# Performance work log

Measured on AMD Instinct MI355X. Metric: run time of the kernel, lower is better.

## Reference

```python
import jax, jax.numpy as jnp
import numpy as np

N_HEADS = 16


def setup_inputs() -> dict:
    key = jax.random.key(0)
    ks = jax.random.split(key, 6)
    b, s, d = 1, 2048, 2048
    x = jax.random.normal(ks[0], (b, s, d), dtype=jnp.float32)
    Wqkv = jax.random.normal(ks[1], (d, 3 * d), dtype=jnp.float32) * (d ** -0.5)
    Wqkv_bias = jax.random.normal(ks[2], (3 * d,), dtype=jnp.float32) * 0.02
    out_w = jax.random.normal(ks[3], (d, d), dtype=jnp.float32) * (d ** -0.5)
    out_b = jax.random.normal(ks[4], (d,), dtype=jnp.float32) * 0.02
    attn_bias = jax.random.normal(ks[5], (1, N_HEADS, 1, s), dtype=jnp.float32)
    key_padding_mask = jnp.ones((b, s), dtype=bool)
    return {"x": x, "Wqkv": Wqkv, "Wqkv_bias": Wqkv_bias, "out_w": out_w,
            "out_b": out_b, "attn_bias": attn_bias,
            "key_padding_mask": key_padding_mask}


def reference(x, Wqkv, Wqkv_bias, out_w, out_b, attn_bias, key_padding_mask):
    b, s, d = x.shape
    h = N_HEADS
    dh = d // h
    qkv = x @ Wqkv + Wqkv_bias                      # [b, s, 3d]
    q, k, v = jnp.split(qkv, 3, axis=-1)
    q = q.reshape(b, s, h, dh).transpose(0, 2, 1, 3)  # b h s d
    k = k.reshape(b, s, h, dh).transpose(0, 2, 1, 3)
    v = v.reshape(b, s, h, dh).transpose(0, 2, 1, 3)
    scale = 1.0 / jnp.sqrt(jnp.asarray(dh, x.dtype))
    attn_weight = jnp.einsum('bhqd,bhkd->bhqk', q, k) * scale
    attn_weight = attn_weight + attn_bias           # broadcast [1,h,1,s]
    min_val = jnp.finfo(x.dtype).min
    # key padding mask: [b, s_k] -> [b,1,1,s_k]
    attn_weight = jnp.where(key_padding_mask[:, None, None, :], attn_weight, min_val)
    # causal mask (s_q == s_k)
    causal = jnp.tril(jnp.ones((s, s), dtype=bool))
    attn_weight = jnp.where(causal[None, None, :, :], attn_weight, min_val)
    attn_weight = jax.nn.softmax(attn_weight, axis=-1)
    out = jnp.einsum('bhqk,bhkd->bhqd', attn_weight, v)
    out = out.transpose(0, 2, 1, 3).reshape(b, s, d)  # b s (h d)
    return out @ out_w + out_b
```

## Files before the change

kernel.cpp:

```cpp
#include <hip/hip_runtime.h>
#include <hip/hip_bf16.h>
#include <stdint.h>


#define SQ 2048
#define DM 2048
#define NH 16
#define DH 128
#define N3 6144
#define QKVN (NH * SQ * DH)

typedef unsigned short u16;
typedef __bf16 bf16_t;
typedef bf16_t bf16x8 __attribute__((ext_vector_type(8)));
typedef float f32x4 __attribute__((ext_vector_type(4)));
typedef const __attribute__((address_space(1))) unsigned int guint;
typedef __attribute__((address_space(3))) unsigned int luint;

__device__ __forceinline__ float b2f(u16 u) {
    union { uint32_t i; float f; } c; c.i = ((uint32_t)u) << 16; return c.f;
}
__device__ __forceinline__ u16 f2b(float f) {
    union { float f; uint32_t i; } c; c.f = f;
    uint32_t r = c.i + 0x7FFF + ((c.i >> 16) & 1);
    return (u16)(r >> 16);
}
__device__ __forceinline__ uint32_t pk(u16 a, u16 b) {
    return (uint32_t)a | ((uint32_t)b << 16);
}
__device__ __forceinline__ uint32_t pkrnd(float a, float b) {
    union { float f; uint32_t i; } x, y; x.f = a; y.f = b;
    return __builtin_amdgcn_perm(y.i + 0x8000u, x.i + 0x8000u, 0x07060302u);
}
__device__ __forceinline__ float ld1(const void* p, size_t i, bool fp32) {
    return fp32 ? ((const float*)p)[i] : b2f(((const u16*)p)[i]);
}

__global__ void detect_dtype(const void* x, int* flag) {
    __shared__ int bad;
    if (threadIdx.x == 0) bad = 0;
    __syncthreads();
    float v = b2f(((const u16*)x)[threadIdx.x]);
    if (!(fabsf(v) <= 1024.0f)) atomicOr(&bad, 1);
    __syncthreads();
    if (threadIdx.x == 0) *flag = bad;
}

__global__ __launch_bounds__(256) void convert_x(
    const void* __restrict__ x, u16* __restrict__ xb, const int* __restrict__ flagp)
{
    const bool fp32 = (*flagp != 0);
    const size_t i = ((size_t)blockIdx.x * 256 + threadIdx.x) * 8;
    uint4 v;
    if (fp32) {
        const float* p = (const float*)x + i;
        float4 a = *(const float4*)p, b = *(const float4*)(p + 4);
        v.x = pkrnd(a.x, a.y); v.y = pkrnd(a.z, a.w);
        v.z = pkrnd(b.x, b.y); v.w = pkrnd(b.z, b.w);
    } else {
        v = *(const uint4*)((const u16*)x + i);
    }
    *(uint4*)(xb + i) = v;
}

__global__ __launch_bounds__(256) void transpose_w(
    const void* __restrict__ W, u16* __restrict__ Wt, int N,
    const int* __restrict__ flagp)
{
    const bool fp32 = (*flagp != 0);
    __shared__ __attribute__((aligned(16))) u16 tile[64 * 72];
    const int t = threadIdx.x;
    const int n0 = blockIdx.x * 64, k0 = blockIdx.y * 64;
#pragma unroll
    for (int i = 0; i < 2; ++i) {
        int c = t + 256 * i; int kr = c >> 3; int n8 = (c & 7) * 8;
        uint4 v;
        if (fp32) {
            const float* p = (const float*)W + (size_t)(k0 + kr) * N + n0 + n8;
            float4 a = *(const float4*)p, b = *(const float4*)(p + 4);
            v.x = pkrnd(a.x, a.y); v.y = pkrnd(a.z, a.w);
            v.z = pkrnd(b.x, b.y); v.w = pkrnd(b.z, b.w);
        } else {
            v = *(const uint4*)((const u16*)W + (size_t)(k0 + kr) * N + n0 + n8);
        }
        *(uint4*)&tile[kr * 72 + n8] = v;
    }
    __syncthreads();
#pragma unroll
    for (int i = 0; i < 2; ++i) {
        int c = t + 256 * i; int nr = c >> 3; int k8 = (c & 7) * 8;
        uint32_t dw[4];
#pragma unroll
        for (int j = 0; j < 4; ++j)
            dw[j] = pk(tile[(k8 + 2*j) * 72 + nr], tile[(k8 + 2*j + 1) * 72 + nr]);
        *(uint4*)&Wt[(size_t)(n0 + nr) * 2048 + k0 + k8] =
            make_uint4(dw[0], dw[1], dw[2], dw[3]);
    }
}

__global__ __launch_bounds__(256, 2) void qkv_gemm4(
    const u16* __restrict__ xb, const u16* __restrict__ Wt,
    const void* __restrict__ bias,
    u16* __restrict__ Q, u16* __restrict__ K, u16* __restrict__ Vt,
    const int* __restrict__ flagp)
{
    const bool fp32 = (*flagp != 0);
    __shared__ __attribute__((aligned(16))) u16 Alds[2][128 * 64];
    __shared__ __attribute__((aligned(16))) u16 Blds[2][192 * 64];
    const int t = threadIdx.x;
    const int w = t >> 6, l = t & 63;
    const int wm = w >> 1, wn = w & 1;
    const int lq = l & 15, quad = l >> 4;
    const int rsub = t >> 3;
    const int sw = ((t & 7) ^ (rsub & 7)) << 3;

    const int orig = blockIdx.x;
    const int xcd = orig & 7, j = orig >> 3;
    const int bx = (xcd & 3) * 8 + (j & 7);
    const int by = (xcd >> 2) * 8 + (j >> 3);
    const int m0 = by * 128, n0 = bx * 192;

    const u16* Ag = xb + (size_t)m0 * 2048;
    const u16* Bg = Wt + (size_t)n0 * 2048;

#define STAGE_A(u, ue) do {                                                   \
    if ((u) < 32) {                                                           \
      _Pragma("unroll")                                                       \
      for (int i_ = 0; i_ < 2; ++i_) {                                        \
        const int rb_ = i_ * 64 + (ue) * 32;                                  \
        const u16* src_ = Ag + (size_t)(rb_ + rsub) * 2048 + (u) * 64 + sw;   \
        __builtin_amdgcn_global_load_lds((guint*)(const void*)src_,           \
          (luint*)(void*)&Alds[(u) & 1][rb_ * 64 + t * 8], 16, 0, 0);         \
      }                                                                       \
    } } while (0)

#define STAGE_B(u) do {                                                       \
    if ((u) < 32) {                                                           \
      _Pragma("unroll")                                                       \
      for (int i_ = 0; i_ < 6; ++i_) {                                        \
        const int rb_ = i_ * 32;                                              \
        const u16* src_ = Bg + (size_t)(rb_ + rsub) * 2048 + (u) * 64 + sw;   \
        __builtin_amdgcn_global_load_lds((guint*)(const void*)src_,           \
          (luint*)(void*)&Blds[(u) & 1][rb_ * 64 + t * 8], 16, 0, 0);         \
      }                                                                       \
    } } while (0)

#define READ_A(buf, mh) do {                                                  \
    _Pragma("unroll")                                                         \
    for (int mf_ = 0; mf_ < 2; ++mf_) {                                       \
      const int r_ = wm*64 + ((mh)*2 + mf_)*16 + lq;                          \
      _Pragma("unroll")                                                       \
      for (int ks_ = 0; ks_ < 2; ++ks_) {                                     \
        const int c_ = (ks_*4 + quad) ^ (r_ & 7);                             \
        a[mf_][ks_] = *(const bf16x8*)&Alds[buf][r_*64 + c_*8];               \
      }                                                                       \
    } } while (0)

#define READ_B(dst, buf, nhh) do {                                            \
    _Pragma("unroll")                                                         \
    for (int nf_ = 0; nf_ < 3; ++nf_) {                                       \
      const int r_ = wn*96 + ((nhh)*3 + nf_)*16 + lq;                         \
      _Pragma("unroll")                                                       \
      for (int ks_ = 0; ks_ < 2; ++ks_) {                                     \
        const int c_ = (ks_*4 + quad) ^ (r_ & 7);                             \
        dst[nf_][ks_] = *(const bf16x8*)&Blds[buf][r_*64 + c_*8];             \
      }                                                                       \
    } } while (0)

#define MMA_Q(mh, nhh, bsrc) do {                                             \
    __builtin_amdgcn_s_setprio(1);                                            \
    _Pragma("unroll")                                                         \
    for (int mf_ = 0; mf_ < 2; ++mf_)                                         \
    _Pragma("unroll")                                                         \
    for (int nf_ = 0; nf_ < 3; ++nf_)                                         \
    _Pragma("unroll")                                                         \
    for (int ks_ = 0; ks_ < 2; ++ks_)                                         \
      acc[(mh)*2+mf_][(nhh)*3+nf_] =                                          \
        __builtin_amdgcn_mfma_f32_16x16x32_bf16(a[mf_][ks_], bsrc[nf_][ks_],  \
          acc[(mh)*2+mf_][(nhh)*3+nf_], 0, 0, 0);                             \
    __builtin_amdgcn_s_setprio(0);                                            \
} while (0)

#define TILE_BODY(T, buf, BEC, BEN) do {                                      \
                                                                      \
    READ_A(buf, 0);                                                           \
    __builtin_amdgcn_s_barrier();                                             \
    asm volatile("s_waitcnt lgkmcnt(0)" ::: "memory");                        \
    MMA_Q(0, 0, BEC);                                                         \
    __builtin_amdgcn_s_barrier();                                             \
                                                                      \
    READ_B(bo, buf, 1);                                                       \
    STAGE_A((T) + 2, 0);                                                      \
    if ((T) >= 30) asm volatile("s_waitcnt vmcnt(0)" ::: "memory");           \
    else           asm volatile("s_waitcnt vmcnt(2)" ::: "memory");           \
    __builtin_amdgcn_s_barrier();                                             \
    asm volatile("s_waitcnt lgkmcnt(0)" ::: "memory");                        \
    MMA_Q(0, 1, bo);                                                          \
    __builtin_amdgcn_s_barrier();                                             \
                                                                      \
    READ_A(buf, 1);                                                           \
    STAGE_B((T) + 2);                                                         \
    __builtin_amdgcn_s_barrier();                                             \
    asm volatile("s_waitcnt lgkmcnt(0)" ::: "memory");                        \
    MMA_Q(1, 1, bo);                                                          \
    __builtin_amdgcn_s_barrier();                                             \
                                                                      \
    READ_B(BEN, (buf) ^ 1, 0);                                                \
    STAGE_A((T) + 2, 1);                                                      \
    __builtin_amdgcn_s_barrier();                                             \
    asm volatile("s_waitcnt lgkmcnt(0)" ::: "memory");                        \
    MMA_Q(1, 0, BEC);                                                         \
    __builtin_amdgcn_s_barrier();                                             \
} while (0)

    const f32x4 vzero = {0.f, 0.f, 0.f, 0.f};
    f32x4 acc[4][6];
#pragma unroll
    for (int i = 0; i < 4; ++i)
#pragma unroll
        for (int j2 = 0; j2 < 6; ++j2) acc[i][j2] = vzero;
    bf16x8 a[2][2], bo[3][2], be_a[3][2], be_b[3][2];

    STAGE_A(0, 0); STAGE_B(0); STAGE_A(0, 1);
    STAGE_A(1, 0); STAGE_B(1); STAGE_A(1, 1);
    asm volatile("s_waitcnt vmcnt(10)" ::: "memory");
    __builtin_amdgcn_s_barrier();
    READ_B(be_a, 0, 0);

#pragma unroll 1
    for (int T = 0; T < 32; T += 2) {
        TILE_BODY(T,     0, be_a, be_b);
        TILE_BODY(T + 1, 1, be_b, be_a);
    }

    const float scale = 0.08838834764831845f;
#pragma unroll
    for (int nf = 0; nf < 6; ++nf) {
        const int n = n0 + wn*96 + nf*16 + lq;
        const float bn = ld1(bias, n, fp32);
        const int which = n >> 11, r2 = n & 2047, h = r2 >> 7, dc = r2 & 127;
#pragma unroll
        for (int mf = 0; mf < 4; ++mf) {
#pragma unroll
            for (int r = 0; r < 4; ++r) {
                const int m = m0 + wm*64 + mf*16 + quad*4 + r;
                const float val = acc[mf][nf][r] + bn;
                if (which == 0)
                    Q[((size_t)(h << 11) + m) * DH + dc] = f2b(val * scale);
                else if (which == 1)
                    K[((size_t)(h << 11) + m) * DH + dc] = f2b(val);
                else {
                    const int kl = m & 63;
                    const int pos = ((kl >> 5) << 5) + (((kl >> 2) & 3) << 3)
                                  + (((kl >> 4) & 1) << 2) + (kl & 3);
                    const int mp = (m & ~63) | pos;
                    Vt[((size_t)h * DH + dc) * SQ + mp] = f2b(val);
                }
            }
        }
    }
#undef STAGE_A
#undef STAGE_B
#undef READ_A
#undef READ_B
#undef MMA_Q
#undef TILE_BODY
}

__global__ __launch_bounds__(256) void attn_mfma(
    const u16* __restrict__ Q, const u16* __restrict__ K,
    const u16* __restrict__ Vt, const void* __restrict__ attn_bias,
    u16* __restrict__ Ob0, u16* __restrict__ Ob1,
    float* __restrict__ Lb0, float* __restrict__ Lb1,
    const int* __restrict__ flagp)
{
    const bool fp32 = (*flagp != 0);
    __shared__ __attribute__((aligned(16))) u16 Qs[4 * 64 * 32];
    __shared__ __attribute__((aligned(16))) u16 Ks[4 * 64 * 32];
    __shared__ __attribute__((aligned(16))) u16 Vs[128 * 64];
    __shared__ __attribute__((aligned(16))) float biasF[2048];

    const int t = threadIdx.x;
    const int w = t >> 6, l = t & 63;
    const int lq = l & 15, quad = l >> 4;
    const int px = blockIdx.x, h = blockIdx.y, par = blockIdx.z;

    const u16* Qh = Q + (size_t)h * SQ * DH;
    const u16* Kh = K + (size_t)h * SQ * DH;
    const u16* Vh = Vt + (size_t)h * DH * SQ;
    u16* Ob = par ? Ob1 : Ob0;
    float* Lb = par ? Lb1 : Lb0;

#pragma unroll
    for (int i = 0; i < 8; ++i) {
        int j = t + 256 * i;
        biasF[j] = ld1(attn_bias, (size_t)h * SQ + j, fp32);
    }

    const f32x4 vzero = {0.f, 0.f, 0.f, 0.f};

    for (int phase = 0; phase < 2; ++phase) {
        const int qt = phase ? (31 - px) : px;
        const int q0 = qt * 64;
        const int qbase = q0 + w * 16;

        __syncthreads();
#pragma unroll
        for (int i = 0; i < 4; ++i) {
            const int ci = w * 4 + i;
            const int kc = ci >> 2, kg = ci & 3;
            const u16* src = Qh + (size_t)(q0 + kg*16 + (l >> 2)) * DH
                           + kc*32 + (l & 3) * 8;
            __builtin_amdgcn_global_load_lds((guint*)(const void*)src,
                (luint*)(void*)&Qs[ci * 512], 16, 0, 0);
        }
        __syncthreads();
        bf16x8 bq[4];
#pragma unroll
        for (int kc = 0; kc < 4; ++kc)
            bq[kc] = *(const bf16x8*)&Qs[kc*2048 + (w*16 + lq)*32 + quad*8];

        f32x4 O[8];
#pragma unroll
        for (int i = 0; i < 8; ++i) O[i] = vzero;
        float lsum = 0.0f;

        for (int kt = par; kt <= qt; kt += 2) {
            const int k0 = kt * 64;
            __syncthreads();
#pragma unroll
            for (int i = 0; i < 4; ++i) {
                const int ci = w * 4 + i;
                const int kc = ci >> 2, kg = ci & 3;
                const u16* src = Kh + (size_t)(k0 + kg*16 + (l >> 2)) * DH
                               + kc*32 + (l & 3) * 8;
                __builtin_amdgcn_global_load_lds((guint*)(const void*)src,
                    (luint*)(void*)&Ks[ci * 512], 16, 0, 0);
            }
#pragma unroll
            for (int i = 0; i < 4; ++i) {
                const int ci = w * 4 + i;
                const int dim = ci * 8 + (l >> 3);
                const u16* src = Vh + (size_t)dim * SQ + k0
                               + (((l & 7) ^ (l >> 3)) << 3);
                __builtin_amdgcn_global_load_lds((guint*)(const void*)src,
                    (luint*)(void*)&Vs[ci * 512], 16, 0, 0);
            }
            __syncthreads();

            f32x4 S[4];
#pragma unroll
            for (int ks = 0; ks < 4; ++ks) S[ks] = vzero;
#pragma unroll
            for (int kc = 0; kc < 4; ++kc) {
#pragma unroll
                for (int ks = 0; ks < 4; ++ks) {
                    bf16x8 ak = *(const bf16x8*)&Ks[kc*2048 + (ks*16 + lq)*32 + quad*8];
                    S[ks] = __builtin_amdgcn_mfma_f32_16x16x32_bf16(ak, bq[kc], S[ks], 0, 0, 0);
                }
            }

            const bool full = (k0 + 63) <= qbase;
            uint32_t Ppk[4][2];
            float part = 0.0f;
#pragma unroll
            for (int ks = 0; ks < 4; ++ks) {
                const f32x4 b4 = *(const f32x4*)&biasF[k0 + ks*16 + quad*4];
                float p[4];
#pragma unroll
                for (int r = 0; r < 4; ++r) {
                    float pe = __expf(S[ks][r] + b4[r]);
                    if (!full) {
                        const int key = k0 + ks*16 + quad*4 + r;
                        if (key > qbase + lq) pe = 0.0f;
                    }
                    p[r] = pe;
                    part += pe;
                }
                Ppk[ks][0] = pkrnd(p[0], p[1]);
                Ppk[ks][1] = pkrnd(p[2], p[3]);
            }
            lsum += part;

#pragma unroll
            for (int s2 = 0; s2 < 2; ++s2) {
                union { uint32_t u[4]; bf16x8 v; } bP;
                bP.u[0] = Ppk[2*s2][0];   bP.u[1] = Ppk[2*s2][1];
                bP.u[2] = Ppk[2*s2+1][0]; bP.u[3] = Ppk[2*s2+1][1];
                const int ch = ((s2*4 + quad) ^ (lq & 7)) << 3;
#pragma unroll
                for (int ds = 0; ds < 8; ++ds) {
                    bf16x8 aV = *(const bf16x8*)&Vs[(ds*16 + lq)*64 + ch];
                    O[ds] = __builtin_amdgcn_mfma_f32_16x16x32_bf16(aV, bP.v, O[ds], 0, 0, 0);
                }
            }
        }

        lsum += __shfl_xor(lsum, 16, 64);
        lsum += __shfl_xor(lsum, 32, 64);
        if (l < 16) Lb[(size_t)h * SQ + qbase + l] = lsum;
        u16* orow = Ob + (size_t)(qbase + lq) * DM + h * DH;
#pragma unroll
        for (int ds = 0; ds < 8; ++ds) {
            uint2 o2;
            o2.x = pkrnd(O[ds][0], O[ds][1]);
            o2.y = pkrnd(O[ds][2], O[ds][3]);
            *(uint2*)&orow[ds*16 + quad*4] = o2;
        }
    }
}

__global__ __launch_bounds__(256) void combine_o(
    const u16* __restrict__ O0, const u16* __restrict__ O1,
    const float* __restrict__ L0, const float* __restrict__ L1,
    u16* __restrict__ attno)
{
    const size_t i = ((size_t)blockIdx.x * 256 + threadIdx.x) * 8;
    const int row = (int)(i >> 11);
    const int h = ((int)i & 2047) >> 7;
    const float inv = 1.0f / (L0[h * SQ + row] + L1[h * SQ + row]);
    const ushort4 a = *(const ushort4*)(O0 + i);
    const ushort4 b = *(const ushort4*)(O1 + i);
    const ushort4 c = *(const ushort4*)(O0 + i + 4);
    const ushort4 d = *(const ushort4*)(O1 + i + 4);
    uint4 v;
    v.x = pkrnd((b2f(a.x)+b2f(b.x))*inv, (b2f(a.y)+b2f(b.y))*inv);
    v.y = pkrnd((b2f(a.z)+b2f(b.z))*inv, (b2f(a.w)+b2f(b.w))*inv);
    v.z = pkrnd((b2f(c.x)+b2f(d.x))*inv, (b2f(c.y)+b2f(d.y))*inv);
    v.w = pkrnd((b2f(c.z)+b2f(d.z))*inv, (b2f(c.w)+b2f(d.w))*inv);
    *(uint4*)(attno + i) = v;
}

__global__ __launch_bounds__(256) void out_gemm(
    const u16* __restrict__ attno, const u16* __restrict__ OWt,
    const void* __restrict__ bias, void* __restrict__ out,
    const int* __restrict__ flagp)
{
    const bool fp32 = (*flagp != 0);
    __shared__ __attribute__((aligned(16))) u16 Alds[128 * 32];
    __shared__ __attribute__((aligned(16))) u16 Blds[64 * 32];
    const int t = threadIdx.x;
    const int m0 = blockIdx.y * 128, n0 = blockIdx.x * 64;
    const int w = t >> 6, l = t & 63;
    const int lq = l & 15, quad = l >> 4;
    const int srow = l >> 2, scol = (l & 3) * 8;
    const f32x4 vzero = {0.f, 0.f, 0.f, 0.f};
    f32x4 acc[2][4];
#pragma unroll
    for (int i = 0; i < 2; ++i)
#pragma unroll
        for (int j = 0; j < 4; ++j) acc[i][j] = vzero;

    for (int k0 = 0; k0 < 2048; k0 += 32) {
#pragma unroll
        for (int i = 0; i < 2; ++i) {
            const int row = w * 32 + i * 16 + srow;
            const u16* ga = attno + (size_t)(m0 + row) * 2048 + k0 + scol;
            __builtin_amdgcn_global_load_lds((guint*)(const void*)ga,
                (luint*)(void*)&Alds[w * 1024 + i * 512], 16, 0, 0);
        }
        {
            const u16* gb = OWt + (size_t)(n0 + w*16 + srow) * 2048 + k0 + scol;
            __builtin_amdgcn_global_load_lds((guint*)(const void*)gb,
                (luint*)(void*)&Blds[w * 512], 16, 0, 0);
        }
        __syncthreads();
        bf16x8 bfr[4];
#pragma unroll
        for (int ns = 0; ns < 4; ++ns)
            bfr[ns] = *(const bf16x8*)&Blds[(ns*16 + lq) * 32 + quad*8];
#pragma unroll
        for (int ms = 0; ms < 2; ++ms) {
            bf16x8 af = *(const bf16x8*)&Alds[(w*32 + ms*16 + lq) * 32 + quad*8];
#pragma unroll
            for (int ns = 0; ns < 4; ++ns)
                acc[ms][ns] = __builtin_amdgcn_mfma_f32_16x16x32_bf16(
                    af, bfr[ns], acc[ms][ns], 0, 0, 0);
        }
        __syncthreads();
    }

#pragma unroll
    for (int ns = 0; ns < 4; ++ns) {
        const int n = n0 + ns*16 + lq;
        const float bn = ld1(bias, n, fp32);
#pragma unroll
        for (int ms = 0; ms < 2; ++ms) {
#pragma unroll
            for (int r = 0; r < 4; ++r) {
                const int m = m0 + w*32 + ms*16 + quad*4 + r;
                const float v = acc[ms][ns][r] + bn;
                const size_t idx = (size_t)m * DM + n;
                if (fp32) ((float*)out)[idx] = v;
                else      ((u16*)out)[idx]  = f2b(v);
            }
        }
    }
}

extern "C" void kernel_launch(void* const* d_in, const int* in_sizes, int n_in,
                              void* d_out, int out_size, void* d_ws, size_t ws_size,
                              hipStream_t stream)
{
    const void* x      = d_in[0];
    const void* wqkv   = d_in[1];
    const void* wqkv_b = d_in[2];
    const void* out_w  = d_in[3];
    const void* out_b  = d_in[4];
    const void* attn_b = d_in[5];

    char* base = (char*)d_ws;
    int* flag = (int*)base;
    u16* xb   = (u16*)(base + 256);
    u16* Wt   = xb + (size_t)SQ * DM;
    u16* Qb   = Wt + (size_t)N3 * DM;
    u16* Kb   = Qb + QKVN;
    u16* Vtb  = Kb + QKVN;
    float* L0 = (float*)(Vtb + QKVN);
    float* L1 = L0 + NH * SQ;
    u16* OWt  = Wt;
    u16* Ob0  = Wt + (size_t)DM * DM;
    u16* Ob1  = Ob0 + (size_t)SQ * DM;
    u16* attno = xb;

    detect_dtype<<<1, 256, 0, stream>>>(x, flag);
    convert_x<<<(SQ * DM) / (256 * 8), 256, 0, stream>>>(x, xb, flag);
    transpose_w<<<dim3(N3/64, DM/64), 256, 0, stream>>>(wqkv, Wt, N3, flag);
    qkv_gemm4<<<dim3(512), 256, 0, stream>>>(xb, Wt, wqkv_b, Qb, Kb, Vtb, flag);
    transpose_w<<<dim3(DM/64, DM/64), 256, 0, stream>>>(out_w, OWt, DM, flag);
    attn_mfma<<<dim3(16, NH, 2), 256, 0, stream>>>(Qb, Kb, Vtb, attn_b,
                                                   Ob0, Ob1, L0, L1, flag);
    combine_o<<<(SQ * DM) / (256 * 8), 256, 0, stream>>>(Ob0, Ob1, L0, L1, attno);
    out_gemm<<<dim3(DM/64, SQ/128), 256, 0, stream>>>(attno, OWt, out_b,
                                                      d_out, flag);
}
```

Measured before the change: 287.4 us.

## Load QKV GEMM B operand directly from global into registers, bypassing LDS

The B (weight) tile in the QKV GEMM is no longer staged through shared memory. Each wave now loads its own 96-column slice straight from global memory into double-buffered registers one k-step ahead, while A keeps its LDS double buffer. The pipeline is restructured from four MMA phases to two per tile, with adjusted vmcnt waits. This removes the B LDS traffic and frees shared memory for occupancy. In exchange it adds register pressure (two 6x2 bf16x8 buffers) and uses uncoalesced, per-lane strided global reads, and waves sharing a column slice load the same weights twice.

```diff
diff --git a/kernel.cpp b/kernel.cpp
--- a/kernel.cpp
+++ b/kernel.cpp
@@ -106,7 +106,6 @@
 {
     const bool fp32 = (*flagp != 0);
     __shared__ __attribute__((aligned(16))) u16 Alds[2][128 * 64];
-    __shared__ __attribute__((aligned(16))) u16 Blds[2][192 * 64];
     const int t = threadIdx.x;
     const int w = t >> 6, l = t & 63;
     const int wm = w >> 1, wn = w & 1;
@@ -121,7 +120,7 @@
     const int m0 = by * 128, n0 = bx * 192;
 
     const u16* Ag = xb + (size_t)m0 * 2048;
-    const u16* Bg = Wt + (size_t)n0 * 2048;
+    const u16* bbase = Wt + (size_t)(n0 + wn * 96 + lq) * 2048 + quad * 8;
 
 #define STAGE_A(u, ue) do {                                                   \
     if ((u) < 32) {                                                           \
@@ -134,15 +133,14 @@
       }                                                                       \
     } } while (0)
 
-#define STAGE_B(u) do {                                                       \
+#define LOAD_B(dst, u) do {                                                   \
     if ((u) < 32) {                                                           \
       _Pragma("unroll")                                                       \
-      for (int i_ = 0; i_ < 6; ++i_) {                                        \
-        const int rb_ = i_ * 32;                                              \
-        const u16* src_ = Bg + (size_t)(rb_ + rsub) * 2048 + (u) * 64 + sw;   \
-        __builtin_amdgcn_global_load_lds((guint*)(const void*)src_,           \
-          (luint*)(void*)&Blds[(u) & 1][rb_ * 64 + t * 8], 16, 0, 0);         \
-      }                                                                       \
+      for (int nf_ = 0; nf_ < 6; ++nf_)                                       \
+        _Pragma("unroll")                                                     \
+        for (int ks_ = 0; ks_ < 2; ++ks_)                                     \
+          dst[nf_][ks_] = *(const bf16x8*)(bbase + (size_t)nf_ * 16 * 2048    \
+                                           + (u) * 64 + ks_ * 32);            \
     } } while (0)
 
 #define READ_A(buf, mh) do {                                                  \
@@ -156,60 +154,40 @@
       }                                                                       \
     } } while (0)
 
-#define READ_B(dst, buf, nhh) do {                                            \
-    _Pragma("unroll")                                                         \
-    for (int nf_ = 0; nf_ < 3; ++nf_) {                                       \
-      const int r_ = wn*96 + ((nhh)*3 + nf_)*16 + lq;                         \
-      _Pragma("unroll")                                                       \
-      for (int ks_ = 0; ks_ < 2; ++ks_) {                                     \
-        const int c_ = (ks_*4 + quad) ^ (r_ & 7);                             \
-        dst[nf_][ks_] = *(const bf16x8*)&Blds[buf][r_*64 + c_*8];             \
-      }                                                                       \
-    } } while (0)
-
-#define MMA_Q(mh, nhh, bsrc) do {                                             \
+#define MMA_Q(mh, bsrc) do {                                                  \
     __builtin_amdgcn_s_setprio(1);                                            \
     _Pragma("unroll")                                                         \
     for (int mf_ = 0; mf_ < 2; ++mf_)                                         \
     _Pragma("unroll")                                                         \
-    for (int nf_ = 0; nf_ < 3; ++nf_)                                         \
+    for (int nf_ = 0; nf_ < 6; ++nf_)                                         \
     _Pragma("unroll")                                                         \
     for (int ks_ = 0; ks_ < 2; ++ks_)                                         \
-      acc[(mh)*2+mf_][(nhh)*3+nf_] =                                          \
+      acc[(mh)*2+mf_][nf_] =                                                  \
         __builtin_amdgcn_mfma_f32_16x16x32_bf16(a[mf_][ks_], bsrc[nf_][ks_],  \
-          acc[(mh)*2+mf_][(nhh)*3+nf_], 0, 0, 0);                             \
+          acc[(mh)*2+mf_][nf_], 0, 0, 0);                                     \
     __builtin_amdgcn_s_setprio(0);                                            \
 } while (0)
 
-#define TILE_BODY(T, buf, BEC, BEN) do {                                      \
+#define TILE_BODY(T, buf, BCUR, BNXT) do {                                    \
                                                                       \
     READ_A(buf, 0);                                                           \
+    STAGE_A((T) + 1, 1);                                                      \
+    asm volatile("" ::: "memory");                  \
+    LOAD_B(BNXT, (T) + 1);                                                    \
+    if ((T) >= 29) asm volatile("s_waitcnt vmcnt(0)" ::: "memory");           \
+    else           asm volatile("s_waitcnt vmcnt(16)" ::: "memory");          \
     __builtin_amdgcn_s_barrier();                                             \
     asm volatile("s_waitcnt lgkmcnt(0)" ::: "memory");                        \
-    MMA_Q(0, 0, BEC);                                                         \
-    __builtin_amdgcn_s_barrier();                                             \
-                                                                      \
-    READ_B(bo, buf, 1);                                                       \
-    STAGE_A((T) + 2, 0);                                                      \
-    if ((T) >= 30) asm volatile("s_waitcnt vmcnt(0)" ::: "memory");           \
-    else           asm volatile("s_waitcnt vmcnt(2)" ::: "memory");           \
-    __builtin_amdgcn_s_barrier();                                             \
-    asm volatile("s_waitcnt lgkmcnt(0)" ::: "memory");                        \
-    MMA_Q(0, 1, bo);                                                          \
+    MMA_Q(0, BCUR);                                                           \
     __builtin_amdgcn_s_barrier();                                             \
                                                                       \
     READ_A(buf, 1);                                                           \
-    STAGE_B((T) + 2);                                                         \
+    STAGE_A((T) + 2, 0);                                                      \
+    if ((T) >= 29) asm volatile("s_waitcnt vmcnt(0)" ::: "memory");           \
+    else           asm volatile("s_waitcnt vmcnt(14)" ::: "memory");          \
     __builtin_amdgcn_s_barrier();                                             \
     asm volatile("s_waitcnt lgkmcnt(0)" ::: "memory");                        \
-    MMA_Q(1, 1, bo);                                                          \
-    __builtin_amdgcn_s_barrier();                                             \
-                                                                      \
-    READ_B(BEN, (buf) ^ 1, 0);                                                \
-    STAGE_A((T) + 2, 1);                                                      \
-    __builtin_amdgcn_s_barrier();                                             \
-    asm volatile("s_waitcnt lgkmcnt(0)" ::: "memory");                        \
-    MMA_Q(1, 0, BEC);                                                         \
+    MMA_Q(1, BCUR);                                                           \
     __builtin_amdgcn_s_barrier();                                             \
 } while (0)
 
@@ -219,18 +197,20 @@
     for (int i = 0; i < 4; ++i)
 #pragma unroll
         for (int j2 = 0; j2 < 6; ++j2) acc[i][j2] = vzero;
-    bf16x8 a[2][2], bo[3][2], be_a[3][2], be_b[3][2];
-
-    STAGE_A(0, 0); STAGE_B(0); STAGE_A(0, 1);
-    STAGE_A(1, 0); STAGE_B(1); STAGE_A(1, 1);
-    asm volatile("s_waitcnt vmcnt(10)" ::: "memory");
+    bf16x8 a[2][2], B_a[6][2], B_b[6][2];
+
+    STAGE_A(0, 0); STAGE_A(0, 1);
+    asm volatile("" ::: "memory");
+    LOAD_B(B_a, 0);
+    asm volatile("" ::: "memory");
+    STAGE_A(1, 0);
+    asm volatile("s_waitcnt vmcnt(14)" ::: "memory");
     __builtin_amdgcn_s_barrier();
-    READ_B(be_a, 0, 0);
 
 #pragma unroll 1
     for (int T = 0; T < 32; T += 2) {
-        TILE_BODY(T,     0, be_a, be_b);
-        TILE_BODY(T + 1, 1, be_b, be_a);
+        TILE_BODY(T,     0, B_a, B_b);
+        TILE_BODY(T + 1, 1, B_b, B_a);
     }
 
     const float scale = 0.08838834764831845f;
@@ -260,9 +240,8 @@
         }
     }
 #undef STAGE_A
-#undef STAGE_B
+#undef LOAD_B
 #undef READ_A
-#undef READ_B
 #undef MMA_Q
 #undef TILE_BODY
 }
```

New measurement: 342.7 us. +19.2%, slower.

## Double-buffer K/V and output GEMM tiles to overlap global loads with MFMA

Applied to the files above, without the earlier changes.

Both the attention kernel and the output projection GEMM now use two LDS buffers. The next K/V tile (or A/B tile) is prefetched with global_load_lds while MFMAs run on the current one, and each iteration ends with a single vmcnt wait plus barrier. In the attention kernel, Q fragments are now read straight from global into registers, so Q no longer passes through LDS. The aim is to hide global-load latency behind compute and remove one barrier per iteration. The cost is doubled LDS use, which may reduce occupancy.

```diff
diff --git a/kernel.cpp b/kernel.cpp
--- a/kernel.cpp
+++ b/kernel.cpp
@@ -275,9 +275,8 @@
     const int* __restrict__ flagp)
 {
     const bool fp32 = (*flagp != 0);
-    __shared__ __attribute__((aligned(16))) u16 Qs[4 * 64 * 32];
-    __shared__ __attribute__((aligned(16))) u16 Ks[4 * 64 * 32];
-    __shared__ __attribute__((aligned(16))) u16 Vs[128 * 64];
+    __shared__ __attribute__((aligned(16))) u16 Ks[2][4 * 64 * 32];
+    __shared__ __attribute__((aligned(16))) u16 Vs[2][128 * 64];
     __shared__ __attribute__((aligned(16))) float biasF[2048];
 
     const int t = threadIdx.x;
@@ -297,6 +296,23 @@
         biasF[j] = ld1(attn_bias, (size_t)h * SQ + j, fp32);
     }
 
+#define STAGE_KV(kt_, b_) do {                                                \
+    const int k0_ = (kt_) * 64;                                               \
+    _Pragma("unroll")                                                         \
+    for (int i_ = 0; i_ < 4; ++i_) {                                          \
+        const int ci_ = w * 4 + i_;                                           \
+        const int kc_ = ci_ >> 2, kg_ = ci_ & 3;                              \
+        const u16* srck_ = Kh + (size_t)(k0_ + kg_*16 + (l >> 2)) * DH        \
+                         + kc_*32 + (l & 3) * 8;                              \
+        __builtin_amdgcn_global_load_lds((guint*)(const void*)srck_,          \
+            (luint*)(void*)&Ks[b_][ci_ * 512], 16, 0, 0);                     \
+        const int dim_ = ci_ * 8 + (l >> 3);                                  \
+        const u16* srcv_ = Vh + (size_t)dim_ * SQ + k0_                       \
+                         + (((l & 7) ^ (l >> 3)) << 3);                       \
+        __builtin_amdgcn_global_load_lds((guint*)(const void*)srcv_,          \
+            (luint*)(void*)&Vs[b_][ci_ * 512], 16, 0, 0);                     \
+    } } while (0)
+
     const f32x4 vzero = {0.f, 0.f, 0.f, 0.f};
 
     for (int phase = 0; phase < 2; ++phase) {
@@ -304,49 +320,26 @@
         const int q0 = qt * 64;
         const int qbase = q0 + w * 16;
 
+        bf16x8 bq[4];
+#pragma unroll
+        for (int kc = 0; kc < 4; ++kc)
+            bq[kc] = *(const bf16x8*)(Qh + (size_t)(qbase + lq) * DH
+                                      + kc*32 + quad*8);
+
         __syncthreads();
-#pragma unroll
-        for (int i = 0; i < 4; ++i) {
-            const int ci = w * 4 + i;
-            const int kc = ci >> 2, kg = ci & 3;
-            const u16* src = Qh + (size_t)(q0 + kg*16 + (l >> 2)) * DH
-                           + kc*32 + (l & 3) * 8;
-            __builtin_amdgcn_global_load_lds((guint*)(const void*)src,
-                (luint*)(void*)&Qs[ci * 512], 16, 0, 0);
-        }
-        __syncthreads();
-        bf16x8 bq[4];
-#pragma unroll
-        for (int kc = 0; kc < 4; ++kc)
-            bq[kc] = *(const bf16x8*)&Qs[kc*2048 + (w*16 + lq)*32 + quad*8];
+        STAGE_KV(par, 0);
+        asm volatile("s_waitcnt vmcnt(0)" ::: "memory");
+        __builtin_amdgcn_s_barrier();
 
         f32x4 O[8];
 #pragma unroll
         for (int i = 0; i < 8; ++i) O[i] = vzero;
         float lsum = 0.0f;
 
+        int buf = 0;
         for (int kt = par; kt <= qt; kt += 2) {
             const int k0 = kt * 64;
-            __syncthreads();
-#pragma unroll
-            for (int i = 0; i < 4; ++i) {
-                const int ci = w * 4 + i;
-                const int kc = ci >> 2, kg = ci & 3;
-                const u16* src = Kh + (size_t)(k0 + kg*16 + (l >> 2)) * DH
-                               + kc*32 + (l & 3) * 8;
-                __builtin_amdgcn_global_load_lds((guint*)(const void*)src,
-                    (luint*)(void*)&Ks[ci * 512], 16, 0, 0);
-            }
-#pragma unroll
-            for (int i = 0; i < 4; ++i) {
-                const int ci = w * 4 + i;
-                const int dim = ci * 8 + (l >> 3);
-                const u16* src = Vh + (size_t)dim * SQ + k0
-                               + (((l & 7) ^ (l >> 3)) << 3);
-                __builtin_amdgcn_global_load_lds((guint*)(const void*)src,
-                    (luint*)(void*)&Vs[ci * 512], 16, 0, 0);
-            }
-            __syncthreads();
+            if (kt + 2 <= qt) STAGE_KV(kt + 2, buf ^ 1);
 
             f32x4 S[4];
 #pragma unroll
@@ -355,7 +348,7 @@
             for (int kc = 0; kc < 4; ++kc) {
 #pragma unroll
                 for (int ks = 0; ks < 4; ++ks) {
-                    bf16x8 ak = *(const bf16x8*)&Ks[kc*2048 + (ks*16 + lq)*32 + quad*8];
+                    bf16x8 ak = *(const bf16x8*)&Ks[buf][kc*2048 + (ks*16 + lq)*32 + quad*8];
                     S[ks] = __builtin_amdgcn_mfma_f32_16x16x32_bf16(ak, bq[kc], S[ks], 0, 0, 0);
                 }
             }
@@ -390,10 +383,14 @@
                 const int ch = ((s2*4 + quad) ^ (lq & 7)) << 3;
 #pragma unroll
                 for (int ds = 0; ds < 8; ++ds) {
-                    bf16x8 aV = *(const bf16x8*)&Vs[(ds*16 + lq)*64 + ch];
+                    bf16x8 aV = *(const bf16x8*)&Vs[buf][(ds*16 + lq)*64 + ch];
                     O[ds] = __builtin_amdgcn_mfma_f32_16x16x32_bf16(aV, bP.v, O[ds], 0, 0, 0);
                 }
             }
+
+            asm volatile("s_waitcnt vmcnt(0)" ::: "memory");
+            __builtin_amdgcn_s_barrier();
+            buf ^= 1;
         }
 
         lsum += __shfl_xor(lsum, 16, 64);
@@ -408,6 +405,7 @@
             *(uint2*)&orow[ds*16 + quad*4] = o2;
         }
     }
+#undef STAGE_KV
 }
 
 __global__ __launch_bounds__(256) void combine_o(
@@ -437,8 +435,8 @@
     const int* __restrict__ flagp)
 {
     const bool fp32 = (*flagp != 0);
-    __shared__ __attribute__((aligned(16))) u16 Alds[128 * 32];
-    __shared__ __attribute__((aligned(16))) u16 Blds[64 * 32];
+    __shared__ __attribute__((aligned(16))) u16 Alds[2][128 * 32];
+    __shared__ __attribute__((aligned(16))) u16 Blds[2][64 * 32];
     const int t = threadIdx.x;
     const int m0 = blockIdx.y * 128, n0 = blockIdx.x * 64;
     const int w = t >> 6, l = t & 63;
@@ -451,34 +449,44 @@
 #pragma unroll
         for (int j = 0; j < 4; ++j) acc[i][j] = vzero;
 
+#define STAGE_OG(k0_, b_) do {                                                \
+    _Pragma("unroll")                                                         \
+    for (int i_ = 0; i_ < 2; ++i_) {                                          \
+        const int row_ = w * 32 + i_ * 16 + srow;                             \
+        const u16* ga_ = attno + (size_t)(m0 + row_) * 2048 + (k0_) + scol;   \
+        __builtin_amdgcn_global_load_lds((guint*)(const void*)ga_,            \
+            (luint*)(void*)&Alds[b_][w * 1024 + i_ * 512], 16, 0, 0);         \
+    }                                                                         \
+    {                                                                         \
+        const u16* gb_ = OWt + (size_t)(n0 + w*16 + srow) * 2048 + (k0_) + scol;\
+        __builtin_amdgcn_global_load_lds((guint*)(const void*)gb_,            \
+            (luint*)(void*)&Blds[b_][w * 512], 16, 0, 0);                     \
+    } } while (0)
+
+    STAGE_OG(0, 0);
+    asm volatile("s_waitcnt vmcnt(0)" ::: "memory");
+    __builtin_amdgcn_s_barrier();
+
+#pragma unroll 1
     for (int k0 = 0; k0 < 2048; k0 += 32) {
-#pragma unroll
-        for (int i = 0; i < 2; ++i) {
-            const int row = w * 32 + i * 16 + srow;
-            const u16* ga = attno + (size_t)(m0 + row) * 2048 + k0 + scol;
-            __builtin_amdgcn_global_load_lds((guint*)(const void*)ga,
-                (luint*)(void*)&Alds[w * 1024 + i * 512], 16, 0, 0);
-        }
-        {
-            const u16* gb = OWt + (size_t)(n0 + w*16 + srow) * 2048 + k0 + scol;
-            __builtin_amdgcn_global_load_lds((guint*)(const void*)gb,
-                (luint*)(void*)&Blds[w * 512], 16, 0, 0);
-        }
-        __syncthreads();
+        const int buf = (k0 >> 5) & 1;
+        if (k0 + 32 < 2048) STAGE_OG(k0 + 32, buf ^ 1);
         bf16x8 bfr[4];
 #pragma unroll
         for (int ns = 0; ns < 4; ++ns)
-            bfr[ns] = *(const bf16x8*)&Blds[(ns*16 + lq) * 32 + quad*8];
+            bfr[ns] = *(const bf16x8*)&Blds[buf][(ns*16 + lq) * 32 + quad*8];
 #pragma unroll
         for (int ms = 0; ms < 2; ++ms) {
-            bf16x8 af = *(const bf16x8*)&Alds[(w*32 + ms*16 + lq) * 32 + quad*8];
+            bf16x8 af = *(const bf16x8*)&Alds[buf][(w*32 + ms*16 + lq) * 32 + quad*8];
 #pragma unroll
             for (int ns = 0; ns < 4; ++ns)
                 acc[ms][ns] = __builtin_amdgcn_mfma_f32_16x16x32_bf16(
                     af, bfr[ns], acc[ms][ns], 0, 0, 0);
         }
-        __syncthreads();
-    }
+        asm volatile("s_waitcnt vmcnt(0)" ::: "memory");
+        __builtin_amdgcn_s_barrier();
+    }
+#undef STAGE_OG
 
 #pragma unroll
     for (int ns = 0; ns < 4; ++ns) {
```

After: 290.0 us. About the same (+0.9%).
